# Kernel tuning notes

Measured on AMD Instinct MI355X. Metric: run time of the kernel, lower is better.

The kernel has to match this reference:

```python
import jax, jax.numpy as jnp
import numpy as np

SEQ, BS, IN, H, NUM_LAYERS = 512, 64, 1024, 1024, 2


def setup_inputs() -> dict:
    key = jax.random.key(0)
    k1, k2, k3, k4 = jax.random.split(key, 4)

    def xavier(k, shape):
        fan_in, fan_out = shape
        lim = jnp.sqrt(6.0 / (fan_in + fan_out))
        return jax.random.uniform(k, shape, jnp.float32, -lim, lim)

    return {
        "x": jax.random.normal(k1, (SEQ, BS, IN), jnp.float32),
        "W_ii0": xavier(k2, (IN, 4 * H)),
        "W_ii": xavier(k3, (H, 4 * H)),
        "W_hi": xavier(k4, (H, 4 * H)),
        "bias": jnp.zeros((4 * H,), jnp.float32),
    }


def _run_layer(x, W_in, W_hi, bias, hidden):
    # x: [seq, bs, feat]; precompute input projection for all timesteps at once
    xw = jnp.einsum('sbf,fg->sbg', x, W_in) + bias  # [seq, bs, 4H]
    bs = x.shape[1]

    def step(carry, xw_t):
        h, c = carry
        gates = xw_t + h @ W_hi  # [bs, 4H]
        i_t = jax.nn.sigmoid(gates[:, :hidden])
        f_t = jax.nn.sigmoid(gates[:, hidden:2 * hidden])
        g_t = jnp.tanh(gates[:, 2 * hidden:3 * hidden])
        o_t = jax.nn.sigmoid(gates[:, 3 * hidden:])
        c = f_t * c + i_t * g_t
        h = o_t * jnp.tanh(c)
        return (h, c), h

    h0 = jnp.zeros((bs, hidden), x.dtype)
    c0 = jnp.zeros((bs, hidden), x.dtype)
    (h, c), hs = jax.lax.scan(step, (h0, c0), xw)
    return hs, h, c  # hs: [seq, bs, hidden]


def reference(x, W_ii0, W_ii, W_hi, bias):
    h = c = None
    for l in range(NUM_LAYERS):
        W_in = W_ii0 if l == 0 else W_ii
        x, h, c = _run_layer(x, W_in, W_hi, bias, H)
    return x, (h, c)
```

## Files before the change

### kernel.cpp

```cpp
#include <hip/hip_runtime.h>

typedef __attribute__((ext_vector_type(8))) short short8;
typedef __attribute__((ext_vector_type(4))) float floatx4;

#define SEQ 512
#define BS  64
#define HID 1024
#define G4  4096
#define NBLK 128
#define NGRP 4
#define BPG  32
#define GBS  16
#define UPB  32

__device__ __forceinline__ unsigned short f2b(float f) {
  union { float f; unsigned u; } v; v.f = f;
  return (unsigned short)((v.u + 0x7FFFu + ((v.u >> 16) & 1u)) >> 16);
}
__device__ __forceinline__ float b2f(unsigned short s) {
  union { unsigned u; float f; } v; v.u = ((unsigned)s) << 16;
  return v.f;
}

__device__ __forceinline__ void gload_lds16_cc(const void* g, void* l) {
  __builtin_amdgcn_global_load_lds(
      (const __attribute__((address_space(1))) unsigned int*)g,
      (__attribute__((address_space(3))) unsigned int*)l,
      16, 0, 17);
}

__global__ void wtrans(const float* __restrict__ W, short* __restrict__ WT) {
  __shared__ float tile[32][33];
  const int tx = threadIdx.x, ty = threadIdx.y;
  const int n0 = blockIdx.x << 5, k0 = blockIdx.y << 5;
#pragma unroll
  for (int i = 0; i < 32; i += 8)
    tile[ty + i][tx] = W[(size_t)(k0 + ty + i) * G4 + n0 + tx];
  __syncthreads();
#pragma unroll
  for (int i = 0; i < 32; i += 8)
    WT[(size_t)(n0 + ty + i) * 1024 + k0 + tx] = (short)f2b(tile[tx][ty + i]);
}

__global__ __launch_bounds__(256)
void conv_bf16(const float* __restrict__ in, unsigned short* __restrict__ out) {
  const size_t i = ((size_t)blockIdx.x * 256 + threadIdx.x) * 8;
  const floatx4 a = *(const floatx4*)(in + i);
  const floatx4 b = *(const floatx4*)(in + i + 4);
  short8 s;
#pragma unroll
  for (int e = 0; e < 4; ++e) { s[e] = (short)f2b(a[e]); s[4 + e] = (short)f2b(b[e]); }
  *(short8*)(out + i) = s;
}

struct FusedArgs {
  const unsigned short* xw;
  const short* wt_hi;
  unsigned short* hbuf;
  float* cbuf;
  unsigned int* flags;
  float* hs;
  unsigned short* hsb;
  float* h_final;
  float* c_final;
  int t0, t1, wr_final;
  const short* A;
  const short* BT;
  const float* bias;
  unsigned short* dst;
  int Mrows, genable;
};

__device__ __forceinline__ void scan_body(const FusedArgs& p, char* smem) {
  float* gsm = (float*)(smem + 32768);
  const int tid = threadIdx.x;
  const int wave = tid >> 6, lane = tid & 63;
  const int lr = lane & 15, lh = lane >> 4;
  const int gate = wave >> 1, uh = wave & 1;
  const int blk = blockIdx.x;
  const int g = blk >> 5;
  const int ub_idx = blk & 31;
  const int gcol = (gate << 10) + ub_idx * UPB + (uh << 4) + lr;

  short8 breg[32];
  {
    const short* wp = p.wt_hi + (size_t)gcol * HID + (lh << 3);
#pragma unroll
    for (int kk = 0; kk < 32; ++kk) breg[kk] = *(const short8*)(wp + (kk << 5));
  }

  const int b_loc = tid >> 5, u_loc = tid & 31;
  const int ci = ((g * GBS + b_loc) << 10) + ub_idx * UPB + u_loc;
  float creg = p.cbuf[ci];

  const int asw = lr & 7;
  const unsigned long long fad =
      (unsigned long long)(p.flags + ((size_t)(g * BPG) + (lane & 31)) * 16);

  for (int t = p.t0; t < p.t1; ++t) {
    float xv[4];
#pragma unroll
    for (int r = 0; r < 4; ++r) {
      const size_t rowi = (size_t)(t - p.t0) * BS + g * GBS + (lh << 2) + r;
      xv[r] = b2f(p.xw[rowi * G4 + gcol]);
    }

    if (t > 0 && wave == 0) {
      unsigned f0;
      for (;;) {
        asm volatile("global_load_dword %0, %1, off sc0 sc1\n\t"
                     "s_waitcnt vmcnt(0)"
                     : "=v"(f0) : "v"(fad) : "memory");
        if (__all(f0 >= (unsigned)t)) break;
        __builtin_amdgcn_s_sleep(1);
      }
    }
    __syncthreads();

    const unsigned short* hb = p.hbuf + (size_t)(t & 1) * (BS * HID) + (size_t)g * GBS * HID;
    unsigned short* hw = p.hbuf + (size_t)((t + 1) & 1) * (BS * HID) + (size_t)g * GBS * HID;

    {
      const int spans[4] = { 2 * wave, 2 * wave + 16, 2 * wave + 1, 2 * wave + 17 };
#pragma unroll
      for (int j = 0; j < 4; ++j) {
        const int i = spans[j];
        const int row = i >> 1, half = i & 1;
        const int chunk = ((half << 6) + lane) ^ (row & 7);
        gload_lds16_cc(hb + row * HID + (chunk << 3), smem + (i << 10));
      }
    }
    asm volatile("s_waitcnt vmcnt(2)" ::: "memory");
    __builtin_amdgcn_s_barrier();
    __builtin_amdgcn_sched_barrier(0);

    floatx4 acc = {0.f, 0.f, 0.f, 0.f};
#pragma unroll
    for (int kk = 0; kk < 16; ++kk) {
      const int kc = (kk << 2) + lh;
      const short8 afr = *(const short8*)(smem + (lr << 11) + ((kc ^ asw) << 4));
      acc = __builtin_amdgcn_mfma_f32_16x16x32_bf16(afr, breg[kk], acc, 0, 0, 0);
    }
    asm volatile("s_waitcnt vmcnt(0)" ::: "memory");
    __builtin_amdgcn_s_barrier();
    __builtin_amdgcn_sched_barrier(0);
#pragma unroll
    for (int kk = 16; kk < 32; ++kk) {
      const int kc = (kk << 2) + lh;
      const short8 afr = *(const short8*)(smem + (lr << 11) + ((kc ^ asw) << 4));
      acc = __builtin_amdgcn_mfma_f32_16x16x32_bf16(afr, breg[kk], acc, 0, 0, 0);
    }

#pragma unroll
    for (int r = 0; r < 4; ++r) {
      const int b = (lh << 2) + r;
      gsm[((gate << 4) + b) * 33 + (uh << 4) + lr] = acc[r] + xv[r];
    }
    __syncthreads();

    const int o = b_loc * 33 + u_loc;
    const float ig = gsm[o];
    const float fg = gsm[16 * 33 + o];
    const float gg2 = gsm[32 * 33 + o];
    const float og = gsm[48 * 33 + o];
    const float iv = 1.f / (1.f + __expf(-ig));
    const float fv = 1.f / (1.f + __expf(-fg));
    const float gv = tanhf(gg2);
    const float ov = 1.f / (1.f + __expf(-og));
    const float cn = fv * creg + iv * gv;
    creg = cn;
    const float hv = ov * tanhf(cn);
    const unsigned hv16 = (unsigned)f2b(hv);
    {
      const unsigned other = (unsigned)__shfl_xor((int)hv16, 1, 64);
      if ((u_loc & 1) == 0) {
        const unsigned val = (hv16 & 0xFFFFu) | (other << 16);
        const unsigned long long dst =
            (unsigned long long)(hw + (size_t)b_loc * HID + ub_idx * UPB + u_loc);
        asm volatile("global_store_dword %0, %1, off sc0 sc1"
                     :: "v"(dst), "v"(val) : "memory");
      }
    }
    asm volatile("s_waitcnt vmcnt(0)" ::: "memory");
    __syncthreads();
    if (tid == 0) {
      const unsigned long long fdst = (unsigned long long)(p.flags + (size_t)blk * 16);
      const unsigned fval = (unsigned)(t + 1);
      asm volatile("global_store_dword %0, %1, off sc0 sc1"
                   :: "v"(fdst), "v"(fval) : "memory");
    }
    {
      const size_t oidx = ((size_t)t * BS + g * GBS + b_loc) * HID + ub_idx * UPB + u_loc;
      p.hs[oidx] = hv;
      p.hsb[oidx] = (unsigned short)hv16;
      if (p.wr_final && t == SEQ - 1) { p.h_final[ci] = hv; p.c_final[ci] = cn; }
    }
  }
  p.cbuf[ci] = creg;
}

__device__ __forceinline__ void gemm_body(const FusedArgs& p, char* smem,
                                          int bi, int gstride) {
  if (!p.genable) return;
  short* Al = (short*)smem;
  short* Bl = (short*)(smem + 10240);
  const int tid = threadIdx.x;
  const int wave = tid >> 6, lane = tid & 63;
  const int lr = lane & 15, lh = lane >> 4;
  const int wm = wave >> 1, wn = wave & 1;
  const int nmt = p.Mrows >> 7;
  const int tot = nmt << 5;
  const int srow = tid >> 2, scol = (tid & 3) << 3;

  for (int tt = bi; tt < tot; tt += gstride) {
    const int m0 = (tt >> 5) << 7, n0 = (tt & 31) << 7;
    const short* aptr = p.A + (size_t)(m0 + srow) * 1024 + scol;
    const short* bptr = p.BT + (size_t)(n0 + srow) * 1024 + scol;
    floatx4 acc[2][4] = {};
    short8 pa = *(const short8*)aptr;
    short8 pb = *(const short8*)bptr;
    for (int it = 0; it < 32; ++it) {
      __syncthreads();
      *(short8*)&Al[srow * 40 + scol] = pa;
      *(short8*)&Bl[srow * 40 + scol] = pb;
      __syncthreads();
      if (it < 31) {
        pa = *(const short8*)(aptr + ((it + 1) << 5));
        pb = *(const short8*)(bptr + ((it + 1) << 5));
      }
      short8 af[2], bf[4];
#pragma unroll
      for (int mt = 0; mt < 2; ++mt)
        af[mt] = *(const short8*)&Al[(wm * 32 + mt * 16 + lr) * 40 + lh * 8];
#pragma unroll
      for (int nt = 0; nt < 4; ++nt)
        bf[nt] = *(const short8*)&Bl[(wn * 64 + nt * 16 + lr) * 40 + lh * 8];
#pragma unroll
      for (int mt = 0; mt < 2; ++mt)
#pragma unroll
        for (int nt = 0; nt < 4; ++nt)
          acc[mt][nt] = __builtin_amdgcn_mfma_f32_16x16x32_bf16(af[mt], bf[nt], acc[mt][nt], 0, 0, 0);
    }
#pragma unroll
    for (int nt = 0; nt < 4; ++nt) {
      const int gc = n0 + wn * 64 + nt * 16 + lr;
      const float bv = p.bias[gc];
#pragma unroll
      for (int mt = 0; mt < 2; ++mt)
#pragma unroll
        for (int r = 0; r < 4; ++r) {
          const int gr = m0 + wm * 32 + mt * 16 + (lh << 2) + r;
          p.dst[(size_t)gr * G4 + gc] = f2b(acc[mt][nt][r] + bv);
        }
    }
  }
}

__global__ __launch_bounds__(512, 2)
void gemm_pre(FusedArgs p) {
  __shared__ __align__(16) char smem[84480];
  gemm_body(p, smem, blockIdx.x, 2 * NBLK);
}

__global__ __launch_bounds__(512, 2)
void lstm_fused(FusedArgs p) {
  __shared__ __align__(16) char smem[84480];
  if (blockIdx.x < NBLK) scan_body(p, smem);
  else                   gemm_body(p, smem, blockIdx.x - NBLK, NBLK);
}

extern "C" void kernel_launch(void* const* d_in, const int* in_sizes, int n_in,
                              void* d_out, int out_size, void* d_ws, size_t ws_size,
                              hipStream_t stream) {
  const float* x    = (const float*)d_in[0];
  const float* Wii0 = (const float*)d_in[1];
  const float* Wii  = (const float*)d_in[2];
  const float* Whi  = (const float*)d_in[3];
  const float* bias = (const float*)d_in[4];
  float* out  = (float*)d_out;
  float* hs   = out;
  float* hfin = out + (size_t)SEQ * BS * HID;
  float* cfin = hfin + BS * HID;

  char* ws = (char*)d_ws;
  short* WT0 = (short*)ws;
  short* WT1 = WT0 + (size_t)G4 * 1024;
  short* WTh = WT1 + (size_t)G4 * 1024;
  unsigned short* hbuf = (unsigned short*)(WTh + (size_t)G4 * 1024);
  float* cbuf = (float*)(hbuf + 2 * BS * HID);
  unsigned int* flags = (unsigned int*)(cbuf + BS * HID);
  unsigned short* xb = (unsigned short*)(flags + NBLK * 16);
  char* tail = (char*)(xb + (size_t)SEQ * BS * HID);
  const size_t head = (size_t)(tail - ws);
  const size_t avail = (ws_size > head) ? ws_size - head : 0;
  const size_t perT = (size_t)BS * G4 * 2;

  int chunk;
  if      (avail >= 2 * 128 * perT) chunk = 128;
  else if (avail >= 2 * 64  * perT) chunk = 64;
  else if (avail >= 2 * 32  * perT) chunk = 32;
  else                              chunk = 8;
  const size_t chunkBytes = (size_t)chunk * perT;
  unsigned short* xwbuf[2] = { (unsigned short*)tail,
                               (unsigned short*)(tail + chunkBytes) };
  const int nc = SEQ / chunk;

  wtrans<<<dim3(128, 32), dim3(32, 8), 0, stream>>>(Wii0, WT0);
  wtrans<<<dim3(128, 32), dim3(32, 8), 0, stream>>>(Wii, WT1);
  wtrans<<<dim3(128, 32), dim3(32, 8), 0, stream>>>(Whi, WTh);
  conv_bf16<<<dim3((SEQ * BS * HID) / (256 * 8)), dim3(256), 0, stream>>>(x, xb);

  for (int layer = 0; layer < 2; ++layer) {
    hipMemsetAsync(hbuf, 0, 2 * BS * HID * sizeof(unsigned short), stream);
    hipMemsetAsync(cbuf, 0, BS * HID * sizeof(float), stream);
    hipMemsetAsync(flags, 0, NBLK * 16 * sizeof(unsigned int), stream);

    if (layer == 0) {
      FusedArgs pa = {};
      pa.A = (const short*)xb;
      pa.BT = WT0;
      pa.bias = bias;
      pa.dst = xwbuf[0];
      pa.Mrows = chunk * BS;
      pa.genable = 1;
      gemm_pre<<<dim3(2 * NBLK), dim3(512), 0, stream>>>(pa);
    }

    for (int c = 0; c < nc; ++c) {
      FusedArgs fa;
      fa.xw = xwbuf[c & 1];
      fa.wt_hi = WTh;
      fa.hbuf = hbuf;
      fa.cbuf = cbuf;
      fa.flags = flags;
      fa.hs = hs;
      fa.hsb = xb;
      fa.h_final = layer ? hfin : nullptr;
      fa.c_final = layer ? cfin : nullptr;
      fa.t0 = c * chunk;
      fa.t1 = (c + 1) * chunk;
      fa.wr_final = layer;
      fa.bias = bias;
      fa.dst = xwbuf[(c + 1) & 1];
      fa.Mrows = chunk * BS;
      const int nxt = ((c + 1) % nc) * chunk * BS;
      fa.A = (const short*)(xb + (size_t)nxt * HID);
      fa.BT = (layer == 0 && c < nc - 1) ? WT0 : WT1;
      fa.genable = !(layer == 1 && c == nc - 1);
      void* args[] = { &fa };
      hipLaunchCooperativeKernel(reinterpret_cast<const void*>(&lstm_fused),
                                 dim3(2 * NBLK), dim3(512), args, 0u, stream);
    }
  }
}
```

Baseline: 3.792 ms.

## Replace per-block flag polling with per-step atomic counters and shuffle-based gate gather

Inter-block synchronization changes from each block writing its own step flag (which waiters poll across 32 flags with a wave vote) to a per-timestep, per-group atomic counter that waiters poll until it reaches the block count. The weight column mapping is also changed so that the four gates of one unit sit in adjacent lanes. They can then be gathered with register shuffles instead of an LDS round trip and an extra block barrier. This shortens the per-step critical path of the recurrent scan, at the cost of atomics on a hot counter and a larger counter array that must be zeroed.

```diff
diff --git a/kernel.cpp b/kernel.cpp
--- a/kernel.cpp
+++ b/kernel.cpp
@@ -58,7 +58,7 @@
   const short* wt_hi;
   unsigned short* hbuf;
   float* cbuf;
-  unsigned int* flags;
+  unsigned int* cnt;
   float* hs;
   unsigned short* hsb;
   float* h_final;
@@ -72,15 +72,14 @@
 };
 
 __device__ __forceinline__ void scan_body(const FusedArgs& p, char* smem) {
-  float* gsm = (float*)(smem + 32768);
   const int tid = threadIdx.x;
   const int wave = tid >> 6, lane = tid & 63;
   const int lr = lane & 15, lh = lane >> 4;
-  const int gate = wave >> 1, uh = wave & 1;
   const int blk = blockIdx.x;
   const int g = blk >> 5;
   const int ub_idx = blk & 31;
-  const int gcol = (gate << 10) + ub_idx * UPB + (uh << 4) + lr;
+  const int u_new = (wave << 2) + (lr >> 2);
+  const int gcol = ((lr & 3) << 10) + ub_idx * UPB + u_new;
 
   short8 breg[32];
   {
@@ -89,13 +88,11 @@
     for (int kk = 0; kk < 32; ++kk) breg[kk] = *(const short8*)(wp + (kk << 5));
   }
 
-  const int b_loc = tid >> 5, u_loc = tid & 31;
-  const int ci = ((g * GBS + b_loc) << 10) + ub_idx * UPB + u_loc;
+  const int b_new = (lh << 2) + (lr & 3);
+  const int ci = ((g * GBS + b_new) << 10) + ub_idx * UPB + u_new;
   float creg = p.cbuf[ci];
-
   const int asw = lr & 7;
-  const unsigned long long fad =
-      (unsigned long long)(p.flags + ((size_t)(g * BPG) + (lane & 31)) * 16);
+  const int j0 = lr & 1, j1 = (lr >> 1) & 1;
 
   for (int t = p.t0; t < p.t1; ++t) {
     float xv[4];
@@ -106,12 +103,14 @@
     }
 
     if (t > 0 && wave == 0) {
+      const unsigned long long cad =
+          (unsigned long long)(p.cnt + ((size_t)t * NGRP + g) * 16);
       unsigned f0;
       for (;;) {
         asm volatile("global_load_dword %0, %1, off sc0 sc1\n\t"
                      "s_waitcnt vmcnt(0)"
-                     : "=v"(f0) : "v"(fad) : "memory");
-        if (__all(f0 >= (unsigned)t)) break;
+                     : "=v"(f0) : "v"(cad) : "memory");
+        if (f0 >= BPG) break;
         __builtin_amdgcn_s_sleep(1);
       }
     }
@@ -151,46 +150,45 @@
       acc = __builtin_amdgcn_mfma_f32_16x16x32_bf16(afr, breg[kk], acc, 0, 0, 0);
     }
 
-#pragma unroll
-    for (int r = 0; r < 4; ++r) {
-      const int b = (lh << 2) + r;
-      gsm[((gate << 4) + b) * 33 + (uh << 4) + lr] = acc[r] + xv[r];
-    }
-    __syncthreads();
-
-    const int o = b_loc * 33 + u_loc;
-    const float ig = gsm[o];
-    const float fg = gsm[16 * 33 + o];
-    const float gg2 = gsm[32 * 33 + o];
-    const float og = gsm[48 * 33 + o];
+    const float x0 = acc[0] + xv[0], x1 = acc[1] + xv[1];
+    const float x2 = acc[2] + xv[2], x3 = acc[3] + xv[3];
+    const float s0 = __shfl_xor(x1, 1), s1 = __shfl_xor(x0, 1);
+    const float s2 = __shfl_xor(x3, 1), s3 = __shfl_xor(x2, 1);
+    const float y0 = j0 ? s0 : x0, y1 = j0 ? x1 : s1;
+    const float y2 = j0 ? s2 : x2, y3 = j0 ? x3 : s3;
+    const float z0s = __shfl_xor(y2, 2), z1s = __shfl_xor(y3, 2);
+    const float z2s = __shfl_xor(y0, 2), z3s = __shfl_xor(y1, 2);
+    const float ig = j1 ? z0s : y0;
+    const float fg = j1 ? z1s : y1;
+    const float gg = j1 ? y2 : z2s;
+    const float og = j1 ? y3 : z3s;
+
     const float iv = 1.f / (1.f + __expf(-ig));
     const float fv = 1.f / (1.f + __expf(-fg));
-    const float gv = tanhf(gg2);
+    const float gv = tanhf(gg);
     const float ov = 1.f / (1.f + __expf(-og));
     const float cn = fv * creg + iv * gv;
     creg = cn;
     const float hv = ov * tanhf(cn);
     const unsigned hv16 = (unsigned)f2b(hv);
+
     {
-      const unsigned other = (unsigned)__shfl_xor((int)hv16, 1, 64);
-      if ((u_loc & 1) == 0) {
+      const unsigned other = (unsigned)__shfl_xor((int)hv16, 4, 64);
+      if ((lr & 4) == 0) {
         const unsigned val = (hv16 & 0xFFFFu) | (other << 16);
         const unsigned long long dst =
-            (unsigned long long)(hw + (size_t)b_loc * HID + ub_idx * UPB + u_loc);
+            (unsigned long long)(hw + (size_t)b_new * HID + ub_idx * UPB + u_new);
         asm volatile("global_store_dword %0, %1, off sc0 sc1"
                      :: "v"(dst), "v"(val) : "memory");
       }
     }
     asm volatile("s_waitcnt vmcnt(0)" ::: "memory");
     __syncthreads();
-    if (tid == 0) {
-      const unsigned long long fdst = (unsigned long long)(p.flags + (size_t)blk * 16);
-      const unsigned fval = (unsigned)(t + 1);
-      asm volatile("global_store_dword %0, %1, off sc0 sc1"
-                   :: "v"(fdst), "v"(fval) : "memory");
-    }
+    if (tid == 0)
+      atomicAdd(p.cnt + ((size_t)(t + 1) * NGRP + g) * 16, 1u);
+
     {
-      const size_t oidx = ((size_t)t * BS + g * GBS + b_loc) * HID + ub_idx * UPB + u_loc;
+      const size_t oidx = ((size_t)t * BS + g * GBS + b_new) * HID + ub_idx * UPB + u_new;
       p.hs[oidx] = hv;
       p.hsb[oidx] = (unsigned short)hv16;
       if (p.wr_final && t == SEQ - 1) { p.h_final[ci] = hv; p.c_final[ci] = cn; }
@@ -288,8 +286,8 @@
   short* WTh = WT1 + (size_t)G4 * 1024;
   unsigned short* hbuf = (unsigned short*)(WTh + (size_t)G4 * 1024);
   float* cbuf = (float*)(hbuf + 2 * BS * HID);
-  unsigned int* flags = (unsigned int*)(cbuf + BS * HID);
-  unsigned short* xb = (unsigned short*)(flags + NBLK * 16);
+  unsigned int* cnt = (unsigned int*)(cbuf + BS * HID);
+  unsigned short* xb = (unsigned short*)(cnt + (size_t)(SEQ + 1) * NGRP * 16);
   char* tail = (char*)(xb + (size_t)SEQ * BS * HID);
   const size_t head = (size_t)(tail - ws);
   const size_t avail = (ws_size > head) ? ws_size - head : 0;
@@ -313,7 +311,7 @@
   for (int layer = 0; layer < 2; ++layer) {
     hipMemsetAsync(hbuf, 0, 2 * BS * HID * sizeof(unsigned short), stream);
     hipMemsetAsync(cbuf, 0, BS * HID * sizeof(float), stream);
-    hipMemsetAsync(flags, 0, NBLK * 16 * sizeof(unsigned int), stream);
+    hipMemsetAsync(cnt, 0, (size_t)(SEQ + 1) * NGRP * 16 * sizeof(unsigned), stream);
 
     if (layer == 0) {
       FusedArgs pa = {};
@@ -332,7 +330,7 @@
       fa.wt_hi = WTh;
       fa.hbuf = hbuf;
       fa.cbuf = cbuf;
-      fa.flags = flags;
+      fa.cnt = cnt;
       fa.hs = hs;
       fa.hsb = xb;
       fa.h_final = layer ? hfin : nullptr;
```

Measured after the change: 4.473 ms. 18.0% more time.

## Split flag polling per wave and store h in k-chunked layout for direct MFMA loads

Applied to the files above, without the earlier changes.

Each wave now polls only the four producer-block flags whose h chunk it loads, instead of wave 0 polling all 32 flags and then a block-wide barrier. The h buffer is written in a chunked layout (per 32-unit block, 16 rows), so each wave copies whole contiguous 1 KB chunks to LDS without swizzling. The MFMA A-fragment read indexes the chunk directly. The two-phase split load/compute overlap is replaced by one wait-all barrier, which trades the partial overlap for finer-grained dependency waits. The unswizzled LDS reads may cause bank conflicts.

```diff
diff --git a/kernel.cpp b/kernel.cpp
--- a/kernel.cpp
+++ b/kernel.cpp
@@ -93,9 +93,8 @@
   const int ci = ((g * GBS + b_loc) << 10) + ub_idx * UPB + u_loc;
   float creg = p.cbuf[ci];
 
-  const int asw = lr & 7;
   const unsigned long long fad =
-      (unsigned long long)(p.flags + ((size_t)(g * BPG) + (lane & 31)) * 16);
+      (unsigned long long)(p.flags + ((size_t)(g * BPG) + (wave << 2) + (lane & 3)) * 16);
 
   for (int t = p.t0; t < p.t1; ++t) {
     float xv[4];
@@ -105,7 +104,7 @@
       xv[r] = b2f(p.xw[rowi * G4 + gcol]);
     }
 
-    if (t > 0 && wave == 0) {
+    if (t > 0) {
       unsigned f0;
       for (;;) {
         asm volatile("global_load_dword %0, %1, off sc0 sc1\n\t"
@@ -115,39 +114,23 @@
         __builtin_amdgcn_s_sleep(1);
       }
     }
-    __syncthreads();
 
     const unsigned short* hb = p.hbuf + (size_t)(t & 1) * (BS * HID) + (size_t)g * GBS * HID;
     unsigned short* hw = p.hbuf + (size_t)((t + 1) & 1) * (BS * HID) + (size_t)g * GBS * HID;
 
-    {
-      const int spans[4] = { 2 * wave, 2 * wave + 16, 2 * wave + 1, 2 * wave + 17 };
-#pragma unroll
-      for (int j = 0; j < 4; ++j) {
-        const int i = spans[j];
-        const int row = i >> 1, half = i & 1;
-        const int chunk = ((half << 6) + lane) ^ (row & 7);
-        gload_lds16_cc(hb + row * HID + (chunk << 3), smem + (i << 10));
-      }
-    }
-    asm volatile("s_waitcnt vmcnt(2)" ::: "memory");
-    __builtin_amdgcn_s_barrier();
-    __builtin_amdgcn_sched_barrier(0);
-
-    floatx4 acc = {0.f, 0.f, 0.f, 0.f};
-#pragma unroll
-    for (int kk = 0; kk < 16; ++kk) {
-      const int kc = (kk << 2) + lh;
-      const short8 afr = *(const short8*)(smem + (lr << 11) + ((kc ^ asw) << 4));
-      acc = __builtin_amdgcn_mfma_f32_16x16x32_bf16(afr, breg[kk], acc, 0, 0, 0);
+#pragma unroll
+    for (int q = 0; q < 4; ++q) {
+      const int pj = (wave << 2) + q;
+      gload_lds16_cc(hb + (pj << 9) + (lane << 3), smem + (pj << 10));
     }
     asm volatile("s_waitcnt vmcnt(0)" ::: "memory");
     __builtin_amdgcn_s_barrier();
     __builtin_amdgcn_sched_barrier(0);
-#pragma unroll
-    for (int kk = 16; kk < 32; ++kk) {
-      const int kc = (kk << 2) + lh;
-      const short8 afr = *(const short8*)(smem + (lr << 11) + ((kc ^ asw) << 4));
+
+    floatx4 acc = {0.f, 0.f, 0.f, 0.f};
+#pragma unroll
+    for (int kk = 0; kk < 32; ++kk) {
+      const short8 afr = *(const short8*)(smem + (kk << 10) + (lr << 6) + (lh << 4));
       acc = __builtin_amdgcn_mfma_f32_16x16x32_bf16(afr, breg[kk], acc, 0, 0, 0);
     }
 
@@ -175,8 +158,8 @@
       const unsigned other = (unsigned)__shfl_xor((int)hv16, 1, 64);
       if ((u_loc & 1) == 0) {
         const unsigned val = (hv16 & 0xFFFFu) | (other << 16);
-        const unsigned long long dst =
-            (unsigned long long)(hw + (size_t)b_loc * HID + ub_idx * UPB + u_loc);
+        const unsigned long long dst = (unsigned long long)
+            (hw + ((size_t)ub_idx << 9) + (b_loc << 5) + u_loc);
         asm volatile("global_store_dword %0, %1, off sc0 sc1"
                      :: "v"(dst), "v"(val) : "memory");
       }
@@ -184,7 +167,8 @@
     asm volatile("s_waitcnt vmcnt(0)" ::: "memory");
     __syncthreads();
     if (tid == 0) {
-      const unsigned long long fdst = (unsigned long long)(p.flags + (size_t)blk * 16);
+      const unsigned long long fdst =
+          (unsigned long long)(p.flags + (size_t)blk * 16);
       const unsigned fval = (unsigned)(t + 1);
       asm volatile("global_store_dword %0, %1, off sc0 sc1"
                    :: "v"(fdst), "v"(fval) : "memory");
```

Measured after the change: 3.905 ms. +3.0%, slower.
